# Kernel tuning notes

Hardware: AMD Instinct MI355X
Metric: run time of the kernel (lower is better)

## Reference

```python
import jax, jax.numpy as jnp
import numpy as np

CODEBOOK_SIZE = 1024
CODEBOOK_DIM = 64
COMMITMENT_WEIGHT = 0.25
DECAY = 0.99
EPS = 1e-5


def setup_inputs() -> dict:
    key = jax.random.key(0)
    k1, k2, k3 = jax.random.split(key, 3)
    B, D, T = 32, CODEBOOK_DIM, 4096
    z = jax.random.normal(k1, (B, D, T), dtype=jnp.float32)
    embedding = jax.random.normal(k2, (CODEBOOK_SIZE, CODEBOOK_DIM), dtype=jnp.float32)
    cluster_size = jnp.zeros((CODEBOOK_SIZE,), dtype=jnp.float32)
    embed_avg = jax.random.normal(k3, (CODEBOOK_SIZE, CODEBOOK_DIM), dtype=jnp.float32)
    return {"z": z, "embedding": embedding, "cluster_size": cluster_size, "embed_avg": embed_avg}


def reference(z, embedding, cluster_size, embed_avg):
    # z: [B, D, T]; embedding/embed_avg: [K, D]; cluster_size: [K]
    B, D, T = z.shape
    K = embedding.shape[0]
    z_flat = jnp.transpose(z, (0, 2, 1)).reshape(-1, D)  # [N, D], N = B*T

    # squared-euclidean distances via expansion (matches torch cdist expansion)
    dist = (
        jnp.sum(z_flat * z_flat, axis=1, keepdims=True)
        + jnp.sum(embedding * embedding, axis=1)
        - 2.0 * (z_flat @ embedding.T)
    )  # [N, K]
    indices = jnp.argmin(dist, axis=1)  # [N] int

    # EMA updates (training path). one_hot.sum(0) -> segment count; one_hot.T @ z_flat -> segment sum
    counts = jax.ops.segment_sum(jnp.ones(z_flat.shape[0], dtype=z_flat.dtype), indices, num_segments=K)
    new_cluster_size = cluster_size * DECAY + (1.0 - DECAY) * counts
    embed_sum = jax.ops.segment_sum(z_flat, indices, num_segments=K)  # [K, D]
    new_embed_avg = embed_avg * DECAY + (1.0 - DECAY) * embed_sum
    n = jnp.sum(new_cluster_size)
    smoothed = (new_cluster_size + EPS) / (n + K * EPS) * n  # Laplace smoothing
    new_embedding = new_embed_avg / smoothed[:, None]  # [K, D]

    # quantize with the *updated* codebook (as in the torch in-place update)
    z_q_flat = new_embedding[indices]  # [N, D] gather
    loss = COMMITMENT_WEIGHT * jnp.mean((z_flat - jax.lax.stop_gradient(z_q_flat)) ** 2)
    # straight-through estimator
    z_q_flat = z_flat + jax.lax.stop_gradient(z_q_flat - z_flat)
    z_q = jnp.transpose(z_q_flat.reshape(B, T, D), (0, 2, 1))  # [B, D, T]
    return z_q, loss, indices.reshape(B, T)
```

## Files before the change

kernel.cpp:

```cpp
#include <hip/hip_runtime.h>

#define N_PTS 131072
#define TD 4096
#define DD 64
#define KK 1024
#define MARGIN_TH 2e-3f
#define BPAD 72

typedef short bf16x8 __attribute__((ext_vector_type(8)));
typedef float f32x4  __attribute__((ext_vector_type(4)));

__device__ inline unsigned short f2bf(float f) {
    unsigned u = __float_as_uint(f);
    unsigned r = u + 0x7FFFu + ((u >> 16) & 1u);
    return (unsigned short)(r >> 16);
}
__device__ inline float bf2f(unsigned short h) {
    return __uint_as_float(((unsigned)h) << 16);
}

__global__ __launch_bounds__(256) void vq_prep(const float* __restrict__ z,
                                               unsigned short* __restrict__ zh,
                                               unsigned short* __restrict__ zl)
{
    __shared__ float tile[64][65];
    const int tid = threadIdx.x;
    const int b = blockIdx.x >> 6;
    const int t0 = (blockIdx.x & 63) * 64;

    const int d = tid >> 2, tq = tid & 3;
#pragma unroll
    for (int it = 0; it < 4; ++it) {
        const int tt = tq * 16 + it * 4;
        const float4 v = *(const float4*)(z + ((size_t)b * DD + d) * TD + t0 + tt);
        tile[d][tt] = v.x; tile[d][tt + 1] = v.y; tile[d][tt + 2] = v.z; tile[d][tt + 3] = v.w;
    }
    __syncthreads();

    const int p = tid >> 2, dg = tid & 3;
    bf16x8 h0, h1, l0, l1;
#pragma unroll
    for (int j = 0; j < 8; ++j) {
        const float v0 = tile[dg * 16 + j][p];
        const unsigned short a = f2bf(v0);
        h0[j] = (short)a; l0[j] = (short)f2bf(v0 - bf2f(a));
        const float v1 = tile[dg * 16 + 8 + j][p];
        const unsigned short c = f2bf(v1);
        h1[j] = (short)c; l1[j] = (short)f2bf(v1 - bf2f(c));
    }
    const size_t o = ((size_t)(b * TD + t0 + p)) * DD + dg * 16;
    *(bf16x8*)(zh + o) = h0;
    *(bf16x8*)(zh + o + 8) = h1;
    *(bf16x8*)(zl + o) = l0;
    *(bf16x8*)(zl + o + 8) = l1;
}

__global__ __launch_bounds__(256) void vq_eprep(const float* __restrict__ emb,
                                                unsigned short* __restrict__ eh,
                                                unsigned short* __restrict__ el,
                                                float* __restrict__ halfnorm)
{
    const int k = blockIdx.x * 256 + threadIdx.x;
    if (k >= KK) return;
    const float* e = emb + (size_t)k * DD;
    double s = 0.0;
#pragma unroll
    for (int d = 0; d < DD; ++d) {
        const float v = e[d];
        const double dv = (double)v;
        s = fma(dv, dv, s);
        const unsigned short h = f2bf(v);
        eh[(size_t)k * DD + d] = h;
        el[(size_t)k * DD + d] = f2bf(v - bf2f(h));
    }
    halfnorm[k] = (float)(0.5 * s);
}

__global__ __launch_bounds__(256, 4) void vq_screen_mfma(
    const unsigned short* __restrict__ zh, const unsigned short* __restrict__ zl,
    const unsigned short* __restrict__ eh, const unsigned short* __restrict__ el,
    const float* __restrict__ hn,
    int* __restrict__ idx_ws, float* __restrict__ ind_out,
    int* __restrict__ nflag, int* __restrict__ flags)
{
    __shared__ __align__(16) unsigned short ehs[2][16 * BPAD];
    __shared__ __align__(16) unsigned short els[2][16 * BPAD];
    __shared__ float hns[2][16];

    const int tid = threadIdx.x;
    const int lane = tid & 63;
    const int wid = tid >> 6;
    const int quad = lane >> 4;
    const int col = lane & 15;
    const int pbase = blockIdx.x * 128 + wid * 32;

    const bf16x8* pA0h = (const bf16x8*)(zh + (size_t)(pbase + col) * DD + quad * 8);
    const bf16x8* pA0l = (const bf16x8*)(zl + (size_t)(pbase + col) * DD + quad * 8);
    const bf16x8* pA1h = (const bf16x8*)(zh + (size_t)(pbase + 16 + col) * DD + quad * 8);
    const bf16x8* pA1l = (const bf16x8*)(zl + (size_t)(pbase + 16 + col) * DD + quad * 8);
    const bf16x8 A0h0 = pA0h[0], A0h1 = pA0h[4];
    const bf16x8 A0l0 = pA0l[0], A0l1 = pA0l[4];
    const bf16x8 A1h0 = pA1h[0], A1h1 = pA1h[4];
    const bf16x8 A1l0 = pA1l[0], A1l1 = pA1l[4];

    const int sidx = tid & 127;
    const int scode = sidx >> 3;
    const int schunk = sidx & 7;
    const bool shi = (tid < 128);
    const unsigned short* sgl = shi ? eh : el;
    const int soff = scode * BPAD + schunk * 8;

    {
        const bf16x8 r = *(const bf16x8*)(sgl + (size_t)scode * DD + schunk * 8);
        *(bf16x8*)((shi ? &ehs[0][0] : &els[0][0]) + soff) = r;
        if (tid < 16) hns[0][tid] = hn[tid];
    }
    __syncthreads();

    float best0[4]  = {1e30f, 1e30f, 1e30f, 1e30f};
    float best20[4] = {1e30f, 1e30f, 1e30f, 1e30f};
    int   bidx0[4]  = {0, 0, 0, 0};
    float best1[4]  = {1e30f, 1e30f, 1e30f, 1e30f};
    float best21[4] = {1e30f, 1e30f, 1e30f, 1e30f};
    int   bidx1[4]  = {0, 0, 0, 0};

    for (int t = 0; t < KK / 16; ++t) {
        const int cur = t & 1;

        bf16x8 nr;
        float nh = 0.f;
        if (t < 63) {
            nr = *(const bf16x8*)(sgl + (size_t)((t + 1) * 16 + scode) * DD + schunk * 8);
            if (tid < 16) nh = hn[(t + 1) * 16 + tid];
        }

        const unsigned short* bh = &ehs[cur][col * BPAD + quad * 8];
        const unsigned short* bl = &els[cur][col * BPAD + quad * 8];
        const bf16x8 Bh0 = *(const bf16x8*)(bh);
        const bf16x8 Bh1 = *(const bf16x8*)(bh + 32);
        const bf16x8 Bl0 = *(const bf16x8*)(bl);
        const bf16x8 Bl1 = *(const bf16x8*)(bl + 32);
        const float hnv = hns[cur][col];

        if (t < 63) {
            *(bf16x8*)((shi ? &ehs[cur ^ 1][0] : &els[cur ^ 1][0]) + soff) = nr;
            if (tid < 16) hns[cur ^ 1][tid] = nh;
        }

        f32x4 p0 = {0.f, 0.f, 0.f, 0.f}, q0 = {0.f, 0.f, 0.f, 0.f};
        f32x4 p1 = {0.f, 0.f, 0.f, 0.f}, q1 = {0.f, 0.f, 0.f, 0.f};
        p0 = __builtin_amdgcn_mfma_f32_16x16x32_bf16(A0h0, Bh0, p0, 0, 0, 0);
        p1 = __builtin_amdgcn_mfma_f32_16x16x32_bf16(A1h0, Bh0, p1, 0, 0, 0);
        q0 = __builtin_amdgcn_mfma_f32_16x16x32_bf16(A0l0, Bh0, q0, 0, 0, 0);
        q1 = __builtin_amdgcn_mfma_f32_16x16x32_bf16(A1l0, Bh0, q1, 0, 0, 0);
        p0 = __builtin_amdgcn_mfma_f32_16x16x32_bf16(A0h1, Bh1, p0, 0, 0, 0);
        p1 = __builtin_amdgcn_mfma_f32_16x16x32_bf16(A1h1, Bh1, p1, 0, 0, 0);
        q0 = __builtin_amdgcn_mfma_f32_16x16x32_bf16(A0l1, Bh1, q0, 0, 0, 0);
        q1 = __builtin_amdgcn_mfma_f32_16x16x32_bf16(A1l1, Bh1, q1, 0, 0, 0);
        p0 = __builtin_amdgcn_mfma_f32_16x16x32_bf16(A0h0, Bl0, p0, 0, 0, 0);
        p1 = __builtin_amdgcn_mfma_f32_16x16x32_bf16(A1h0, Bl0, p1, 0, 0, 0);
        q0 = __builtin_amdgcn_mfma_f32_16x16x32_bf16(A0h1, Bl1, q0, 0, 0, 0);
        q1 = __builtin_amdgcn_mfma_f32_16x16x32_bf16(A1h1, Bl1, q1, 0, 0, 0);

        const int code = t * 16 + col;
#pragma unroll
        for (int r = 0; r < 4; ++r) {
            const float s0 = hnv - (p0[r] + q0[r]);
            const bool l0 = s0 < best0[r];
            best20[r] = fminf(best20[r], fmaxf(best0[r], s0));
            best0[r] = l0 ? s0 : best0[r];
            bidx0[r] = l0 ? code : bidx0[r];
            const float s1 = hnv - (p1[r] + q1[r]);
            const bool l1 = s1 < best1[r];
            best21[r] = fminf(best21[r], fmaxf(best1[r], s1));
            best1[r] = l1 ? s1 : best1[r];
            bidx1[r] = l1 ? code : bidx1[r];
        }

        __syncthreads();
    }

#pragma unroll
    for (int off = 1; off < 16; off <<= 1) {
#pragma unroll
        for (int r = 0; r < 4; ++r) {
            {
                const float ob  = __shfl_xor(best0[r],  off, 64);
                const float ob2 = __shfl_xor(best20[r], off, 64);
                const int   oi  = __shfl_xor(bidx0[r],  off, 64);
                const float nb2 = fminf(fminf(best20[r], ob2), fmaxf(best0[r], ob));
                if (ob < best0[r]) { best0[r] = ob; bidx0[r] = oi; }
                best20[r] = nb2;
            }
            {
                const float ob  = __shfl_xor(best1[r],  off, 64);
                const float ob2 = __shfl_xor(best21[r], off, 64);
                const int   oi  = __shfl_xor(bidx1[r],  off, 64);
                const float nb2 = fminf(fminf(best21[r], ob2), fmaxf(best1[r], ob));
                if (ob < best1[r]) { best1[r] = ob; bidx1[r] = oi; }
                best21[r] = nb2;
            }
        }
    }

    if (col == 0) {
#pragma unroll
        for (int r = 0; r < 4; ++r) {
            const int n0 = pbase + quad * 4 + r;
            idx_ws[n0] = bidx0[r];
            ind_out[n0] = (float)bidx0[r];
            if (best20[r] - best0[r] < MARGIN_TH) {
                const int pos = atomicAdd(nflag, 1);
                flags[pos] = n0;
            }
            const int n1 = pbase + 16 + quad * 4 + r;
            idx_ws[n1] = bidx1[r];
            ind_out[n1] = (float)bidx1[r];
            if (best21[r] - best1[r] < MARGIN_TH) {
                const int pos = atomicAdd(nflag, 1);
                flags[pos] = n1;
            }
        }
    }
}

__global__ __launch_bounds__(256) void vq_fallback(
    const float* __restrict__ z, const float* __restrict__ emb,
    int* __restrict__ idx_ws, float* __restrict__ ind_out,
    const int* __restrict__ nflag, const int* __restrict__ flags)
{
    __shared__ float zs[4][DD];
    const int total = *nflag;
    const int lane = threadIdx.x & 63;
    const int wid = threadIdx.x >> 6;
    const int gw = blockIdx.x * 4 + wid;

    for (int i = gw; i < total; i += gridDim.x * 4) {
        const int n = flags[i];
        const int b = n >> 12, t = n & 4095;
        zs[wid][lane] = z[((size_t)b * DD + lane) * TD + t];
        __builtin_amdgcn_s_waitcnt(0);
        double best = 1e300;
        int bi = KK;
        for (int kc = 0; kc < KK / 64; ++kc) {
            const int k = kc * 64 + lane;
            const float4* e = (const float4*)(emb + (size_t)k * DD);
            double dot = 0.0, nn = 0.0;
#pragma unroll
            for (int j = 0; j < 16; ++j) {
                float4 ev = e[j];
                double e0 = (double)ev.x, e1 = (double)ev.y, e2 = (double)ev.z, e3 = (double)ev.w;
                nn = fma(e0, e0, fma(e1, e1, fma(e2, e2, fma(e3, e3, nn))));
                dot = fma((double)zs[wid][4 * j + 0], e0,
                      fma((double)zs[wid][4 * j + 1], e1,
                      fma((double)zs[wid][4 * j + 2], e2,
                      fma((double)zs[wid][4 * j + 3], e3, dot))));
            }
            double s = 0.5 * nn - dot;
            if (s < best || (s == best && k < bi)) { best = s; bi = k; }
        }
        for (int off = 32; off > 0; off >>= 1) {
            double os = __shfl_down(best, off, 64);
            int oi = __shfl_down(bi, off, 64);
            if (os < best || (os == best && oi < bi)) { best = os; bi = oi; }
        }
        if (lane == 0) { idx_ws[n] = bi; ind_out[n] = (float)bi; }
    }
}

__global__ __launch_bounds__(256) void vq_hist(const int* __restrict__ idx_ws, int* __restrict__ hist)
{
    __shared__ int h[KK];
    for (int i = threadIdx.x; i < KK; i += 256) h[i] = 0;
    __syncthreads();
    const int base = blockIdx.x * 2048;
#pragma unroll
    for (int j = 0; j < 8; ++j)
        atomicAdd(&h[idx_ws[base + j * 256 + threadIdx.x]], 1);
    __syncthreads();
    for (int i = threadIdx.x; i < KK; i += 256)
        if (h[i]) atomicAdd(&hist[i], h[i]);
}

__global__ __launch_bounds__(1024) void vq_prefix_smo(
    const int* __restrict__ hist, const float* __restrict__ cs,
    int* __restrict__ cursor, float* __restrict__ rsmo)
{
    __shared__ int tmp[KK];
    __shared__ double dred[KK];
    const int k = threadIdx.x;
    const int c = hist[k];
    tmp[k] = c;
    const double ncs = 0.99 * (double)cs[k] + 0.01 * (double)c;
    dred[k] = ncs;
    __syncthreads();
    for (int off = 1; off < KK; off <<= 1) {
        int u = (k >= off) ? tmp[k - off] : 0;
        __syncthreads();
        tmp[k] += u;
        __syncthreads();
    }
    cursor[k] = tmp[k] - c;
    for (int s = 512; s > 0; s >>= 1) {
        if (k < s) dred[k] += dred[k + s];
        __syncthreads();
    }
    const double nsum = dred[0];
    const double smo = (ncs + 1e-5) / (nsum + (double)KK * 1e-5) * nsum;
    rsmo[k] = (float)(1.0 / smo);
}

__global__ __launch_bounds__(256) void vq_scatter(const int* __restrict__ idx_ws,
                                                  int* __restrict__ cursor, int* __restrict__ order)
{
    const int n = blockIdx.x * 256 + threadIdx.x;
    const int bi = idx_ws[n];
    const int pos = atomicAdd(&cursor[bi], 1);
    order[pos] = n;
}

__global__ __launch_bounds__(256) void vq_esum2(
    const unsigned short* __restrict__ zh, const unsigned short* __restrict__ zl,
    const int* __restrict__ idx_ws, const int* __restrict__ order,
    float* __restrict__ esum)
{
    const int tid = threadIdx.x;
    const int lane = tid & 63;
    const int w = tid >> 6;
    const int base = blockIdx.x * 256 + w * 64;

    const int pid_l = order[base + lane];
    const int code_l = idx_ws[pid_l];

    float v[64];
#pragma unroll
    for (int j = 0; j < 64; ++j) {
        const int pj = __shfl(pid_l, j, 64);
        const size_t o = (size_t)pj * DD + lane;
        v[j] = bf2f(zh[o]) + bf2f(zl[o]);
    }

    float racc = 0.f;
    int cur = __shfl(code_l, 0, 64);
#pragma unroll
    for (int j = 0; j < 64; ++j) {
        const int cj = __shfl(code_l, j, 64);
        if (cj != cur) {
            atomicAdd(&esum[(size_t)cur * DD + lane], racc);
            racc = 0.f;
            cur = cj;
        }
        racc += v[j];
    }
    atomicAdd(&esum[(size_t)cur * DD + lane], racc);
}

__global__ __launch_bounds__(256) void vq_newE(
    const float* __restrict__ avg, const float* __restrict__ esum,
    const float* __restrict__ rsmo, float* __restrict__ newE)
{
    const int j = blockIdx.x * 256 + threadIdx.x;
    newE[j] = (float)((0.99 * (double)avg[j] + 0.01 * (double)esum[j]) * (double)rsmo[j >> 6]);
}

__global__ __launch_bounds__(256) void vq_gather_loss(
    const float* __restrict__ z, const float* __restrict__ newE,
    const int* __restrict__ idx_ws, float* __restrict__ zq_out,
    double* __restrict__ loss_acc, int* __restrict__ done_cnt,
    float* __restrict__ loss_out)
{
    const int tid = threadIdx.x;
    const int n = blockIdx.x * 256 + tid;
    const int b = n >> 12;
    const int t = n & 4095;
    const float* zb = z + ((size_t)b * DD) * TD + t;
    float* ob = zq_out + ((size_t)b * DD) * TD + t;
    const int bi = idx_ws[n];
    const float* e = newE + (size_t)bi * DD;
    double acc = 0.0;
#pragma unroll
    for (int d = 0; d < DD; ++d) {
        float q = e[d];
        float zv = zb[(size_t)d * TD];
        ob[(size_t)d * TD] = q;
        float df = zv - q;
        acc = fma((double)df, (double)df, acc);
    }
    for (int off = 32; off > 0; off >>= 1) acc += __shfl_down(acc, off, 64);
    __shared__ double wsum[4];
    const int wid = tid >> 6, lane = tid & 63;
    if (lane == 0) wsum[wid] = acc;
    __syncthreads();
    if (tid == 0) {
        atomicAdd(loss_acc, wsum[0] + wsum[1] + wsum[2] + wsum[3]);
        __threadfence();
        const int prev = atomicAdd(done_cnt, 1);
        if (prev == gridDim.x - 1) {
            __threadfence();
            *loss_out = (float)(0.25 * (*loss_acc) / (double)(N_PTS * DD));
        }
    }
}

extern "C" void kernel_launch(void* const* d_in, const int* in_sizes, int n_in,
                              void* d_out, int out_size, void* d_ws, size_t ws_size,
                              hipStream_t stream) {
    const float* z    = (const float*)d_in[0];
    const float* emb  = (const float*)d_in[1];
    const float* cs   = (const float*)d_in[2];
    const float* avg  = (const float*)d_in[3];

    float* out      = (float*)d_out;
    float* zq_out   = out;
    float* loss_out = out + 8388608;
    float* ind_out  = out + 8388609;

    unsigned short* zh = (unsigned short*)d_out;
    unsigned short* zl = (unsigned short*)((char*)d_out + 16777216);

    char* ws = (char*)d_ws;
    int*            idx_ws   = (int*)ws;
    float*          newE     = (float*)(ws + 524288);
    float*          esum     = (float*)(ws + 786432);
    int*            hist     = (int*)(ws + 1048576);
    int*            nflag    = (int*)(ws + 1052672);
    int*            done_cnt = (int*)(ws + 1052676);
    double*         loss_acc = (double*)(ws + 1052680);
    float*          halfnorm = (float*)(ws + 1052688);
    int*            cursor   = (int*)(ws + 1056784);
    int*            flags    = (int*)(ws + 1060880);
    int*            order    = (int*)(ws + 1585168);
    unsigned short* eh       = (unsigned short*)(ws + 2109456);
    unsigned short* el       = (unsigned short*)(ws + 2240528);
    float*          rsmo     = (float*)(ws + 2371600);

    hipMemsetAsync(ws + 786432, 0, 266256, stream);

    vq_prep<<<2048, 256, 0, stream>>>(z, zh, zl);
    vq_eprep<<<4, 256, 0, stream>>>(emb, eh, el, halfnorm);
    vq_screen_mfma<<<1024, 256, 0, stream>>>(zh, zl, eh, el, halfnorm,
                                             idx_ws, ind_out, nflag, flags);
    vq_fallback<<<128, 256, 0, stream>>>(z, emb, idx_ws, ind_out, nflag, flags);
    vq_hist<<<64, 256, 0, stream>>>(idx_ws, hist);
    vq_prefix_smo<<<1, 1024, 0, stream>>>(hist, cs, cursor, rsmo);
    vq_scatter<<<N_PTS / 256, 256, 0, stream>>>(idx_ws, cursor, order);
    vq_esum2<<<N_PTS / 256, 256, 0, stream>>>(zh, zl, idx_ws, order, esum);
    vq_newE<<<256, 256, 0, stream>>>(avg, esum, rsmo, newE);
    vq_gather_loss<<<N_PTS / 256, 256, 0, stream>>>(z, newE, idx_ws, zq_out,
                                                    loss_acc, done_cnt, loss_out);
}
```

Before: 303.1 us.

## Fuse prep, fallback, histogram and newE kernels to cut launch count

The codebook prep moves into extra blocks of the z prep kernel. The exact-fp64 fallback for near-tie points now runs inside the MFMA screening kernel, with per-wave masks in place of a global flag list. The histogram is built with global atomics at index-write time, and the newE computation is folded into the gather/loss kernel. The screening kernel moves to 512-thread blocks where only half the threads stage the codebook. The aim is to drop four kernel launches and their intermediate round trips. In exchange it adds global atomic contention on the histogram, serialises fallback work inside screening waves, and recomputes the EMA embedding per point in gather.

```diff
diff --git a/kernel.cpp b/kernel.cpp
--- a/kernel.cpp
+++ b/kernel.cpp
@@ -20,11 +20,33 @@
 }
 
 __global__ __launch_bounds__(256) void vq_prep(const float* __restrict__ z,
+                                               const float* __restrict__ emb,
                                                unsigned short* __restrict__ zh,
-                                               unsigned short* __restrict__ zl)
+                                               unsigned short* __restrict__ zl,
+                                               unsigned short* __restrict__ eh,
+                                               unsigned short* __restrict__ el,
+                                               float* __restrict__ halfnorm)
 {
     __shared__ float tile[64][65];
     const int tid = threadIdx.x;
+
+    if (blockIdx.x >= 2048) {
+        const int k = (blockIdx.x - 2048) * 256 + tid;
+        const float* e = emb + (size_t)k * DD;
+        double s = 0.0;
+#pragma unroll
+        for (int d = 0; d < DD; ++d) {
+            const float v = e[d];
+            const double dv = (double)v;
+            s = fma(dv, dv, s);
+            const unsigned short h = f2bf(v);
+            eh[(size_t)k * DD + d] = h;
+            el[(size_t)k * DD + d] = f2bf(v - bf2f(h));
+        }
+        halfnorm[k] = (float)(0.5 * s);
+        return;
+    }
+
     const int b = blockIdx.x >> 6;
     const int t0 = (blockIdx.x & 63) * 64;
 
@@ -55,44 +77,24 @@
     *(bf16x8*)(zl + o + 8) = l1;
 }
 
-__global__ __launch_bounds__(256) void vq_eprep(const float* __restrict__ emb,
-                                                unsigned short* __restrict__ eh,
-                                                unsigned short* __restrict__ el,
-                                                float* __restrict__ halfnorm)
-{
-    const int k = blockIdx.x * 256 + threadIdx.x;
-    if (k >= KK) return;
-    const float* e = emb + (size_t)k * DD;
-    double s = 0.0;
-#pragma unroll
-    for (int d = 0; d < DD; ++d) {
-        const float v = e[d];
-        const double dv = (double)v;
-        s = fma(dv, dv, s);
-        const unsigned short h = f2bf(v);
-        eh[(size_t)k * DD + d] = h;
-        el[(size_t)k * DD + d] = f2bf(v - bf2f(h));
-    }
-    halfnorm[k] = (float)(0.5 * s);
-}
-
-__global__ __launch_bounds__(256, 4) void vq_screen_mfma(
+__global__ __launch_bounds__(512, 2) void vq_screen_mfma(
     const unsigned short* __restrict__ zh, const unsigned short* __restrict__ zl,
     const unsigned short* __restrict__ eh, const unsigned short* __restrict__ el,
     const float* __restrict__ hn,
-    int* __restrict__ idx_ws, float* __restrict__ ind_out,
-    int* __restrict__ nflag, int* __restrict__ flags)
+    const float* __restrict__ z, const float* __restrict__ emb,
+    int* __restrict__ idx_ws, float* __restrict__ ind_out, int* __restrict__ hist)
 {
     __shared__ __align__(16) unsigned short ehs[2][16 * BPAD];
     __shared__ __align__(16) unsigned short els[2][16 * BPAD];
     __shared__ float hns[2][16];
+    __shared__ float zsf[8][DD];
 
     const int tid = threadIdx.x;
     const int lane = tid & 63;
     const int wid = tid >> 6;
     const int quad = lane >> 4;
     const int col = lane & 15;
-    const int pbase = blockIdx.x * 128 + wid * 32;
+    const int pbase = blockIdx.x * 256 + wid * 32;
 
     const bf16x8* pA0h = (const bf16x8*)(zh + (size_t)(pbase + col) * DD + quad * 8);
     const bf16x8* pA0l = (const bf16x8*)(zl + (size_t)(pbase + col) * DD + quad * 8);
@@ -107,14 +109,15 @@
     const int scode = sidx >> 3;
     const int schunk = sidx & 7;
     const bool shi = (tid < 128);
+    const bool stg = (tid < 256);
     const unsigned short* sgl = shi ? eh : el;
     const int soff = scode * BPAD + schunk * 8;
 
-    {
+    if (stg) {
         const bf16x8 r = *(const bf16x8*)(sgl + (size_t)scode * DD + schunk * 8);
         *(bf16x8*)((shi ? &ehs[0][0] : &els[0][0]) + soff) = r;
-        if (tid < 16) hns[0][tid] = hn[tid];
-    }
+    }
+    if (tid < 16) hns[0][tid] = hn[tid];
     __syncthreads();
 
     float best0[4]  = {1e30f, 1e30f, 1e30f, 1e30f};
@@ -129,10 +132,9 @@
 
         bf16x8 nr;
         float nh = 0.f;
-        if (t < 63) {
+        if (t < 63 && stg)
             nr = *(const bf16x8*)(sgl + (size_t)((t + 1) * 16 + scode) * DD + schunk * 8);
-            if (tid < 16) nh = hn[(t + 1) * 16 + tid];
-        }
+        if (t < 63 && tid < 16) nh = hn[(t + 1) * 16 + tid];
 
         const unsigned short* bh = &ehs[cur][col * BPAD + quad * 8];
         const unsigned short* bl = &els[cur][col * BPAD + quad * 8];
@@ -142,10 +144,9 @@
         const bf16x8 Bl1 = *(const bf16x8*)(bl + 32);
         const float hnv = hns[cur][col];
 
-        if (t < 63) {
+        if (t < 63 && stg)
             *(bf16x8*)((shi ? &ehs[cur ^ 1][0] : &els[cur ^ 1][0]) + soff) = nr;
-            if (tid < 16) hns[cur ^ 1][tid] = nh;
-        }
+        if (t < 63 && tid < 16) hns[cur ^ 1][tid] = nh;
 
         f32x4 p0 = {0.f, 0.f, 0.f, 0.f}, q0 = {0.f, 0.f, 0.f, 0.f};
         f32x4 p1 = {0.f, 0.f, 0.f, 0.f}, q1 = {0.f, 0.f, 0.f, 0.f};
@@ -203,42 +204,36 @@
         }
     }
 
+    unsigned mflag = 0;
     if (col == 0) {
 #pragma unroll
         for (int r = 0; r < 4; ++r) {
-            const int n0 = pbase + quad * 4 + r;
-            idx_ws[n0] = bidx0[r];
-            ind_out[n0] = (float)bidx0[r];
-            if (best20[r] - best0[r] < MARGIN_TH) {
-                const int pos = atomicAdd(nflag, 1);
-                flags[pos] = n0;
+            if (best20[r] - best0[r] < MARGIN_TH) mflag |= 1u << (quad * 4 + r);
+            else {
+                const int n0 = pbase + quad * 4 + r;
+                idx_ws[n0] = bidx0[r];
+                ind_out[n0] = (float)bidx0[r];
+                atomicAdd(&hist[bidx0[r]], 1);
             }
-            const int n1 = pbase + 16 + quad * 4 + r;
-            idx_ws[n1] = bidx1[r];
-            ind_out[n1] = (float)bidx1[r];
-            if (best21[r] - best1[r] < MARGIN_TH) {
-                const int pos = atomicAdd(nflag, 1);
-                flags[pos] = n1;
+            if (best21[r] - best1[r] < MARGIN_TH) mflag |= 1u << (16 + quad * 4 + r);
+            else {
+                const int n1 = pbase + 16 + quad * 4 + r;
+                idx_ws[n1] = bidx1[r];
+                ind_out[n1] = (float)bidx1[r];
+                atomicAdd(&hist[bidx1[r]], 1);
             }
         }
     }
-}
-
-__global__ __launch_bounds__(256) void vq_fallback(
-    const float* __restrict__ z, const float* __restrict__ emb,
-    int* __restrict__ idx_ws, float* __restrict__ ind_out,
-    const int* __restrict__ nflag, const int* __restrict__ flags)
-{
-    __shared__ float zs[4][DD];
-    const int total = *nflag;
-    const int lane = threadIdx.x & 63;
-    const int wid = threadIdx.x >> 6;
-    const int gw = blockIdx.x * 4 + wid;
-
-    for (int i = gw; i < total; i += gridDim.x * 4) {
-        const int n = flags[i];
-        const int b = n >> 12, t = n & 4095;
-        zs[wid][lane] = z[((size_t)b * DD + lane) * TD + t];
+    mflag |= __shfl_xor(mflag, 16, 64);
+    mflag |= __shfl_xor(mflag, 32, 64);
+    mflag = __shfl(mflag, 0, 64);
+
+    while (mflag) {
+        const int s = __ffs(mflag) - 1;
+        mflag &= mflag - 1;
+        const int pt = pbase + (s & 16) + (s & 15);
+        const int b = pt >> 12, tt = pt & 4095;
+        zsf[wid][lane] = z[((size_t)b * DD + lane) * TD + tt];
         __builtin_amdgcn_s_waitcnt(0);
         double best = 1e300;
         int bi = KK;
@@ -251,35 +246,25 @@
                 float4 ev = e[j];
                 double e0 = (double)ev.x, e1 = (double)ev.y, e2 = (double)ev.z, e3 = (double)ev.w;
                 nn = fma(e0, e0, fma(e1, e1, fma(e2, e2, fma(e3, e3, nn))));
-                dot = fma((double)zs[wid][4 * j + 0], e0,
-                      fma((double)zs[wid][4 * j + 1], e1,
-                      fma((double)zs[wid][4 * j + 2], e2,
-                      fma((double)zs[wid][4 * j + 3], e3, dot))));
+                dot = fma((double)zsf[wid][4 * j + 0], e0,
+                      fma((double)zsf[wid][4 * j + 1], e1,
+                      fma((double)zsf[wid][4 * j + 2], e2,
+                      fma((double)zsf[wid][4 * j + 3], e3, dot))));
             }
-            double s = 0.5 * nn - dot;
-            if (s < best || (s == best && k < bi)) { best = s; bi = k; }
+            double sc = 0.5 * nn - dot;
+            if (sc < best || (sc == best && k < bi)) { best = sc; bi = k; }
         }
         for (int off = 32; off > 0; off >>= 1) {
             double os = __shfl_down(best, off, 64);
             int oi = __shfl_down(bi, off, 64);
             if (os < best || (os == best && oi < bi)) { best = os; bi = oi; }
         }
-        if (lane == 0) { idx_ws[n] = bi; ind_out[n] = (float)bi; }
-    }
-}
-
-__global__ __launch_bounds__(256) void vq_hist(const int* __restrict__ idx_ws, int* __restrict__ hist)
-{
-    __shared__ int h[KK];
-    for (int i = threadIdx.x; i < KK; i += 256) h[i] = 0;
-    __syncthreads();
-    const int base = blockIdx.x * 2048;
-#pragma unroll
-    for (int j = 0; j < 8; ++j)
-        atomicAdd(&h[idx_ws[base + j * 256 + threadIdx.x]], 1);
-    __syncthreads();
-    for (int i = threadIdx.x; i < KK; i += 256)
-        if (h[i]) atomicAdd(&hist[i], h[i]);
+        if (lane == 0) {
+            idx_ws[pt] = bi;
+            ind_out[pt] = (float)bi;
+            atomicAdd(&hist[bi], 1);
+        }
+    }
 }
 
 __global__ __launch_bounds__(1024) void vq_prefix_smo(
@@ -355,16 +340,9 @@
     atomicAdd(&esum[(size_t)cur * DD + lane], racc);
 }
 
-__global__ __launch_bounds__(256) void vq_newE(
-    const float* __restrict__ avg, const float* __restrict__ esum,
-    const float* __restrict__ rsmo, float* __restrict__ newE)
-{
-    const int j = blockIdx.x * 256 + threadIdx.x;
-    newE[j] = (float)((0.99 * (double)avg[j] + 0.01 * (double)esum[j]) * (double)rsmo[j >> 6]);
-}
-
 __global__ __launch_bounds__(256) void vq_gather_loss(
-    const float* __restrict__ z, const float* __restrict__ newE,
+    const float* __restrict__ z, const float* __restrict__ avg,
+    const float* __restrict__ esum, const float* __restrict__ rsmo,
     const int* __restrict__ idx_ws, float* __restrict__ zq_out,
     double* __restrict__ loss_acc, int* __restrict__ done_cnt,
     float* __restrict__ loss_out)
@@ -376,14 +354,16 @@
     const float* zb = z + ((size_t)b * DD) * TD + t;
     float* ob = zq_out + ((size_t)b * DD) * TD + t;
     const int bi = idx_ws[n];
-    const float* e = newE + (size_t)bi * DD;
+    const double rs = (double)rsmo[bi];
+    const float* av = avg + (size_t)bi * DD;
+    const float* es = esum + (size_t)bi * DD;
     double acc = 0.0;
 #pragma unroll
     for (int d = 0; d < DD; ++d) {
-        float q = e[d];
-        float zv = zb[(size_t)d * TD];
+        const float q = (float)((0.99 * (double)av[d] + 0.01 * (double)es[d]) * rs);
+        const float zv = zb[(size_t)d * TD];
         ob[(size_t)d * TD] = q;
-        float df = zv - q;
+        const float df = zv - q;
         acc = fma((double)df, (double)df, acc);
     }
     for (int off = 32; off > 0; off >>= 1) acc += __shfl_down(acc, off, 64);
@@ -420,15 +400,12 @@
 
     char* ws = (char*)d_ws;
     int*            idx_ws   = (int*)ws;
-    float*          newE     = (float*)(ws + 524288);
     float*          esum     = (float*)(ws + 786432);
     int*            hist     = (int*)(ws + 1048576);
-    int*            nflag    = (int*)(ws + 1052672);
     int*            done_cnt = (int*)(ws + 1052676);
     double*         loss_acc = (double*)(ws + 1052680);
     float*          halfnorm = (float*)(ws + 1052688);
     int*            cursor   = (int*)(ws + 1056784);
-    int*            flags    = (int*)(ws + 1060880);
     int*            order    = (int*)(ws + 1585168);
     unsigned short* eh       = (unsigned short*)(ws + 2109456);
     unsigned short* el       = (unsigned short*)(ws + 2240528);
@@ -436,16 +413,12 @@
 
     hipMemsetAsync(ws + 786432, 0, 266256, stream);
 
-    vq_prep<<<2048, 256, 0, stream>>>(z, zh, zl);
-    vq_eprep<<<4, 256, 0, stream>>>(emb, eh, el, halfnorm);
-    vq_screen_mfma<<<1024, 256, 0, stream>>>(zh, zl, eh, el, halfnorm,
-                                             idx_ws, ind_out, nflag, flags);
-    vq_fallback<<<128, 256, 0, stream>>>(z, emb, idx_ws, ind_out, nflag, flags);
-    vq_hist<<<64, 256, 0, stream>>>(idx_ws, hist);
+    vq_prep<<<2052, 256, 0, stream>>>(z, emb, zh, zl, eh, el, halfnorm);
+    vq_screen_mfma<<<512, 512, 0, stream>>>(zh, zl, eh, el, halfnorm, z, emb,
+                                            idx_ws, ind_out, hist);
     vq_prefix_smo<<<1, 1024, 0, stream>>>(hist, cs, cursor, rsmo);
     vq_scatter<<<N_PTS / 256, 256, 0, stream>>>(idx_ws, cursor, order);
     vq_esum2<<<N_PTS / 256, 256, 0, stream>>>(zh, zl, idx_ws, order, esum);
-    vq_newE<<<256, 256, 0, stream>>>(avg, esum, rsmo, newE);
-    vq_gather_loss<<<N_PTS / 256, 256, 0, stream>>>(z, newE, idx_ws, zq_out,
+    vq_gather_loss<<<N_PTS / 256, 256, 0, stream>>>(z, avg, esum, rsmo, idx_ws, zq_out,
                                                     loss_acc, done_cnt, loss_out);
 }
```

Result: slower. 346.0 us (+14.2%).
